# Kernel optimization log

Hardware: AMD Instinct MI355X
Metric: run time of the kernel (lower is better)

The kernel has to match this reference:

```python
import jax, jax.numpy as jnp
import numpy as np


def setup_inputs() -> dict:
    key = jax.random.key(0)
    ks = jax.random.split(key, 7)
    B, I, H, O, T = 1024, 2048, 2048, 2048, 30
    s = 1.0 / np.sqrt(H)
    return {
        "x": jax.random.normal(ks[0], (B, I), dtype=jnp.float32),
        "w_ih": jax.random.uniform(ks[1], (3 * H, I), jnp.float32, -s, s),
        "w_hh": jax.random.uniform(ks[2], (3 * H, H), jnp.float32, -s, s),
        "b_ih": jax.random.uniform(ks[3], (3 * H,), jnp.float32, -s, s),
        "b_hh": jax.random.uniform(ks[4], (3 * H,), jnp.float32, -s, s),
        "w_cls": jax.random.uniform(ks[5], (O, H), jnp.float32, -s, s),
        "b_cls": jax.random.uniform(ks[6], (O,), jnp.float32, -s, s),
        "num_timesteps": T,
    }


def reference(x, w_ih, w_hh, b_ih, b_hh, w_cls, b_cls, num_timesteps):
    # Original module never updates hidden_unit inside the loop, so every
    # timestep computes GRUCell(x, 0) -> identical output. Compute once,
    # broadcast across T (same math as the torch loop).
    # GRUCell with h=0: W_hh @ h vanishes; only bias_hh contributes.
    gi = x @ w_ih.T + b_ih                      # [B, 3H]
    i_r, i_z, i_n = jnp.split(gi, 3, axis=1)    # each [B, H]
    h_r, h_z, h_n = jnp.split(b_hh, 3)          # each [H]
    r = jax.nn.sigmoid(i_r + h_r)
    z = jax.nn.sigmoid(i_z + h_z)
    n = jnp.tanh(i_n + r * h_n)
    h_new = (1.0 - z) * n                       # + z * 0
    out = jax.nn.sigmoid(h_new @ w_cls.T + b_cls)  # [B, O]
    B, O = out.shape
    # torch stacks along dim 2 -> [B, O, T]; squeeze is a no-op for B,O,T > 1
    return jnp.broadcast_to(out[:, :, None], (B, O, num_timesteps))
```

## Files before the change

kernel.cpp:

```cpp
#include <hip/hip_runtime.h>
#include <hip/hip_bf16.h>
#include <math.h>

typedef __attribute__((ext_vector_type(8))) _Float16 f16x8;
typedef __attribute__((ext_vector_type(4))) float f32x4;

static __device__ __forceinline__ float sigmoidf_(float x) {
    return 1.0f / (1.0f + expf(-x));
}

__global__ void cvt_swz(const float* __restrict__ src, _Float16* __restrict__ dst,
                        int nchunks, int ck)
{
    const int c = blockIdx.x * 256 + threadIdx.x;
    if (c >= nchunks) return;
    const int row = c / ck;
    const int kc  = c - row * ck;
    const int kcs = (kc & ~7) | ((kc & 7) ^ (row & 7));
    const float* s = src + (size_t)c * 8;
    float4 v0 = *(const float4*)s;
    float4 v1 = *(const float4*)(s + 4);
    f16x8 h;
    h[0] = (_Float16)v0.x; h[1] = (_Float16)v0.y;
    h[2] = (_Float16)v0.z; h[3] = (_Float16)v0.w;
    h[4] = (_Float16)v1.x; h[5] = (_Float16)v1.y;
    h[6] = (_Float16)v1.z; h[7] = (_Float16)v1.w;
    *(f16x8*)(dst + (size_t)row * ((size_t)ck * 8) + (size_t)kcs * 8) = h;
}

template <int BM, int BN, int EPI>
__launch_bounds__(256, 3)
__global__ void gemm16(const _Float16* __restrict__ A, const _Float16* __restrict__ Bw,
                       const float* __restrict__ bias, float* __restrict__ C,
                       int M, int N, int K)
{
    constexpr int BK = 64;
    constexpr int WM = BM / 2, WN = BN / 2;
    constexpr int MR = WM / 16, NR = WN / 16;

    __shared__ _Float16 As[BM * BK];
    __shared__ _Float16 Bs[BN * BK];

    const int tid  = threadIdx.x;
    const int lane = tid & 63;
    const int wid  = tid >> 6;
    const int wr   = wid >> 1;
    const int wc   = wid & 1;
    const int brow = blockIdx.y * BM;
    const int bcol = blockIdx.x * BN;
    const int lr   = lane & 15;
    const int kb   = lane >> 4;

    f32x4 acc[MR][NR] = {};

    for (int k0 = 0; k0 < K; k0 += BK) {
        __syncthreads();
#pragma unroll
        for (int i = 0; i < BM * 8; i += 256) {
            const int c = tid + i;
            const _Float16* src = A + (size_t)(brow + (c >> 3)) * K + k0 + (c & 7) * 8;
            __builtin_amdgcn_global_load_lds(
                (const __attribute__((address_space(1))) void*)src,
                (__attribute__((address_space(3))) void*)&As[(size_t)(i + wid * 64) * 8],
                16, 0, 0);
        }
#pragma unroll
        for (int i = 0; i < BN * 8; i += 256) {
            const int c = tid + i;
            const _Float16* src = Bw + (size_t)(bcol + (c >> 3)) * K + k0 + (c & 7) * 8;
            __builtin_amdgcn_global_load_lds(
                (const __attribute__((address_space(1))) void*)src,
                (__attribute__((address_space(3))) void*)&Bs[(size_t)(i + wid * 64) * 8],
                16, 0, 0);
        }
        __syncthreads();

#pragma unroll
        for (int ks = 0; ks < 2; ++ks) {
            f16x8 af[MR], bf[NR];
#pragma unroll
            for (int m = 0; m < MR; ++m) {
                const int row = wr * WM + m * 16 + lr;
                const int ch  = (ks * 4 + kb) ^ (row & 7);
                af[m] = *(const f16x8*)&As[row * BK + ch * 8];
            }
#pragma unroll
            for (int n = 0; n < NR; ++n) {
                const int row = wc * WN + n * 16 + lr;
                const int ch  = (ks * 4 + kb) ^ (row & 7);
                bf[n] = *(const f16x8*)&Bs[row * BK + ch * 8];
            }
#pragma unroll
            for (int m = 0; m < MR; ++m)
#pragma unroll
                for (int n = 0; n < NR; ++n)
                    acc[m][n] = __builtin_amdgcn_mfma_f32_16x16x32_f16(af[m], bf[n], acc[m][n], 0, 0, 0);
        }
    }

#pragma unroll
    for (int m = 0; m < MR; ++m) {
        const int row0 = brow + wr * WM + m * 16 + (lane >> 4) * 4;
#pragma unroll
        for (int n = 0; n < NR; ++n) {
            const int col = bcol + wc * WN + n * 16 + lr;
            const float bv = bias[col];
#pragma unroll
            for (int j = 0; j < 4; ++j) {
                float v = acc[m][n][j] + bv;
                if (EPI) v = sigmoidf_(v);
                C[(size_t)(row0 + j) * N + col] = v;
            }
        }
    }
}

__global__ void gate_swz(const float* __restrict__ gi, const float* __restrict__ b_hh,
                         _Float16* __restrict__ hn, int B, int H)
{
    const int ch = H >> 3;
    const int c = blockIdx.x * 256 + threadIdx.x;
    if (c >= B * ch) return;
    const int b  = c / ch;
    const int hc = c - b * ch;
    const int h0 = hc * 8;
    const float* g = gi + (size_t)b * 3 * H;
    f16x8 o;
#pragma unroll
    for (int q = 0; q < 2; ++q) {
        float4 ir  = *(const float4*)(g + h0 + 4 * q);
        float4 iz  = *(const float4*)(g + H + h0 + 4 * q);
        float4 in4 = *(const float4*)(g + 2 * H + h0 + 4 * q);
        float4 hr  = *(const float4*)(b_hh + h0 + 4 * q);
        float4 hz  = *(const float4*)(b_hh + H + h0 + 4 * q);
        float4 hn4 = *(const float4*)(b_hh + 2 * H + h0 + 4 * q);
        float r, z;
        r = sigmoidf_(ir.x + hr.x); z = sigmoidf_(iz.x + hz.x);
        o[4 * q + 0] = (_Float16)((1.0f - z) * tanhf(in4.x + r * hn4.x));
        r = sigmoidf_(ir.y + hr.y); z = sigmoidf_(iz.y + hz.y);
        o[4 * q + 1] = (_Float16)((1.0f - z) * tanhf(in4.y + r * hn4.y));
        r = sigmoidf_(ir.z + hr.z); z = sigmoidf_(iz.z + hz.z);
        o[4 * q + 2] = (_Float16)((1.0f - z) * tanhf(in4.z + r * hn4.z));
        r = sigmoidf_(ir.w + hr.w); z = sigmoidf_(iz.w + hz.w);
        o[4 * q + 3] = (_Float16)((1.0f - z) * tanhf(in4.w + r * hn4.w));
    }
    const int hcs = (hc & ~7) | ((hc & 7) ^ (b & 7));
    *(f16x8*)(hn + (size_t)b * H + (size_t)hcs * 8) = o;
}

__global__ void bcast_kernel(const float* __restrict__ res,
                             float* __restrict__ out, int BO, int T)
{
    const int bo0 = blockIdx.x * 256;
    if (T & 1) {
        float* op = out + (size_t)bo0 * T;
        const int n = 256 * T;
        for (int j = threadIdx.x; j < n; j += blockDim.x)
            op[j] = res[bo0 + j / T];
    } else {
        const int half = T >> 1;
        float2* o2 = (float2*)(out + (size_t)bo0 * T);
        const int n2 = 256 * half;
        for (int j = threadIdx.x; j < n2; j += blockDim.x) {
            const float v = res[bo0 + j / half];
            o2[j] = make_float2(v, v);
        }
    }
}

extern "C" void kernel_launch(void* const* d_in, const int* in_sizes, int n_in,
                              void* d_out, int out_size, void* d_ws, size_t ws_size,
                              hipStream_t stream)
{
    const float* x     = (const float*)d_in[0];
    const float* w_ih  = (const float*)d_in[1];
    const float* b_ih  = (const float*)d_in[3];
    const float* b_hh  = (const float*)d_in[4];
    const float* w_cls = (const float*)d_in[5];
    const float* b_cls = (const float*)d_in[6];

    const int H3 = in_sizes[3];
    const int H  = H3 / 3;
    const int I  = in_sizes[1] / H3;
    const int B  = in_sizes[0] / I;
    const int O  = in_sizes[6];
    const int T  = out_size / (B * O);

    _Float16* x16    = (_Float16*)d_ws;
    _Float16* wcls16 = x16 + (size_t)B * I;
    _Float16* hn16   = wcls16 + (size_t)O * H;
    float*    res    = (float*)(hn16 + (size_t)B * H);

    char*     outc  = (char*)d_out;
    _Float16* wih16 = (_Float16*)outc;
    float*    gi    = (float*)(outc + (size_t)H3 * I * 2);
    float*    out   = (float*)d_out;

    dim3 blk(256);

    cvt_swz<<<(B * I / 8 + 255) / 256, blk, 0, stream>>>(x, x16, B * I / 8, I / 8);
    cvt_swz<<<(H3 * I / 8 + 255) / 256, blk, 0, stream>>>(w_ih, wih16, H3 * I / 8, I / 8);
    cvt_swz<<<(O * H / 8 + 255) / 256, blk, 0, stream>>>(w_cls, wcls16, O * H / 8, H / 8);

    gemm16<64, 128, 0><<<dim3(H3 / 128, B / 64), blk, 0, stream>>>(x16, wih16, b_ih, gi, B, H3, I);

    gate_swz<<<(B * H / 8 + 255) / 256, blk, 0, stream>>>(gi, b_hh, hn16, B, H);

    gemm16<64, 64, 1><<<dim3(O / 64, B / 64), blk, 0, stream>>>(hn16, wcls16, b_cls, res, B, O, H);

    bcast_kernel<<<(B * O) / 256, blk, 0, stream>>>(res, out, B * O, T);
}
```

Baseline: 408.9 us.

## Rewrite GEMMs as single-wave double-buffered kernels, fuse broadcast and conversions

The three fp32-to-fp16 conversions are merged into one launch. Both GEMMs are replaced by a single-wavefront (64-thread) kernel that double-buffers LDS tiles with async global-to-LDS loads and raises scheduling priority around the MFMA block. The intermediate gate activations are stored as fp16 to halve their traffic. The classifier GEMM epilogue writes the T-broadcast output directly, which removes the separate broadcast kernel. The trade-offs are lower occupancy per block, a wide uncoalesced strided store in the epilogue, and reduced precision on the intermediate activations.

```diff
diff --git a/kernel.cpp b/kernel.cpp
--- a/kernel.cpp
+++ b/kernel.cpp
@@ -9,113 +9,149 @@
     return 1.0f / (1.0f + expf(-x));
 }
 
-__global__ void cvt_swz(const float* __restrict__ src, _Float16* __restrict__ dst,
-                        int nchunks, int ck)
-{
-    const int c = blockIdx.x * 256 + threadIdx.x;
-    if (c >= nchunks) return;
+__global__ void cvt_all(const float* __restrict__ s0, _Float16* __restrict__ d0, int n0,
+                        const float* __restrict__ s1, _Float16* __restrict__ d1, int n1,
+                        const float* __restrict__ s2, _Float16* __restrict__ d2, int n2,
+                        int ck01, int ck2)
+{
+    int c = blockIdx.x * 256 + threadIdx.x;
+    const float* s; _Float16* d; int ck;
+    if (c < n0)            { s = s0; d = d0; ck = ck01; }
+    else if (c < n0 + n1)  { c -= n0; s = s1; d = d1; ck = ck01; }
+    else                   { c -= n0 + n1; if (c >= n2) return; s = s2; d = d2; ck = ck2; }
     const int row = c / ck;
     const int kc  = c - row * ck;
     const int kcs = (kc & ~7) | ((kc & 7) ^ (row & 7));
-    const float* s = src + (size_t)c * 8;
-    float4 v0 = *(const float4*)s;
-    float4 v1 = *(const float4*)(s + 4);
+    const float* sp = s + (size_t)c * 8;
+    float4 v0 = *(const float4*)sp;
+    float4 v1 = *(const float4*)(sp + 4);
     f16x8 h;
     h[0] = (_Float16)v0.x; h[1] = (_Float16)v0.y;
     h[2] = (_Float16)v0.z; h[3] = (_Float16)v0.w;
     h[4] = (_Float16)v1.x; h[5] = (_Float16)v1.y;
     h[6] = (_Float16)v1.z; h[7] = (_Float16)v1.w;
-    *(f16x8*)(dst + (size_t)row * ((size_t)ck * 8) + (size_t)kcs * 8) = h;
+    *(f16x8*)(d + (size_t)row * ((size_t)ck * 8) + (size_t)kcs * 8) = h;
 }
 
 template <int BM, int BN, int EPI>
-__launch_bounds__(256, 3)
-__global__ void gemm16(const _Float16* __restrict__ A, const _Float16* __restrict__ Bw,
-                       const float* __restrict__ bias, float* __restrict__ C,
-                       int M, int N, int K)
-{
-    constexpr int BK = 64;
-    constexpr int WM = BM / 2, WN = BN / 2;
-    constexpr int MR = WM / 16, NR = WN / 16;
-
-    __shared__ _Float16 As[BM * BK];
-    __shared__ _Float16 Bs[BN * BK];
+__launch_bounds__(64, 1)
+__global__ void gemm_sw(const _Float16* __restrict__ A, const _Float16* __restrict__ Bw,
+                        const float* __restrict__ bias, void* __restrict__ Cv,
+                        int N, int K, int T)
+{
+    constexpr int MR = BM / 16, NR = BN / 16;
+    constexpr int NA = BM / 8, NB = BN / 8;
+    constexpr int NL = NA + NB;
+
+    __shared__ _Float16 As[2][BM * 64];
+    __shared__ _Float16 Bs[2][BN * 64];
 
     const int tid  = threadIdx.x;
-    const int lane = tid & 63;
-    const int wid  = tid >> 6;
-    const int wr   = wid >> 1;
-    const int wc   = wid & 1;
+    const int lr   = tid & 15;
+    const int kb   = tid >> 4;
     const int brow = blockIdx.y * BM;
     const int bcol = blockIdx.x * BN;
-    const int lr   = lane & 15;
-    const int kb   = lane >> 4;
+
+    const _Float16* ap = A  + (size_t)(brow + (tid >> 3)) * K + (tid & 7) * 8;
+    const _Float16* bp = Bw + (size_t)(bcol + (tid >> 3)) * K + (tid & 7) * 8;
+
+    const int eb0 = lr * 64 + (((0 * 4 + kb) ^ (lr & 7)) * 8);
+    const int eb1 = lr * 64 + (((1 * 4 + kb) ^ (lr & 7)) * 8);
 
     f32x4 acc[MR][NR] = {};
 
-    for (int k0 = 0; k0 < K; k0 += BK) {
-        __syncthreads();
-#pragma unroll
-        for (int i = 0; i < BM * 8; i += 256) {
-            const int c = tid + i;
-            const _Float16* src = A + (size_t)(brow + (c >> 3)) * K + k0 + (c & 7) * 8;
+    auto stage = [&](int buf, int kt) {
+        const _Float16* a = ap + (size_t)kt * 64;
+#pragma unroll
+        for (int i = 0; i < NA; ++i)
             __builtin_amdgcn_global_load_lds(
-                (const __attribute__((address_space(1))) void*)src,
-                (__attribute__((address_space(3))) void*)&As[(size_t)(i + wid * 64) * 8],
+                (const __attribute__((address_space(1))) void*)(a + (size_t)i * 8 * K),
+                (__attribute__((address_space(3))) void*)&As[buf][(i * 64 + tid) * 8],
                 16, 0, 0);
-        }
-#pragma unroll
-        for (int i = 0; i < BN * 8; i += 256) {
-            const int c = tid + i;
-            const _Float16* src = Bw + (size_t)(bcol + (c >> 3)) * K + k0 + (c & 7) * 8;
+        const _Float16* b = bp + (size_t)kt * 64;
+#pragma unroll
+        for (int i = 0; i < NB; ++i)
             __builtin_amdgcn_global_load_lds(
-                (const __attribute__((address_space(1))) void*)src,
-                (__attribute__((address_space(3))) void*)&Bs[(size_t)(i + wid * 64) * 8],
+                (const __attribute__((address_space(1))) void*)(b + (size_t)i * 8 * K),
+                (__attribute__((address_space(3))) void*)&Bs[buf][(i * 64 + tid) * 8],
                 16, 0, 0);
-        }
-        __syncthreads();
-
+    };
+
+    auto compute = [&](int cur) {
+        const _Float16* as = &As[cur][0];
+        const _Float16* bs = &Bs[cur][0];
+        __builtin_amdgcn_s_setprio(1);
 #pragma unroll
         for (int ks = 0; ks < 2; ++ks) {
+            const int eb = ks ? eb1 : eb0;
             f16x8 af[MR], bf[NR];
 #pragma unroll
-            for (int m = 0; m < MR; ++m) {
-                const int row = wr * WM + m * 16 + lr;
-                const int ch  = (ks * 4 + kb) ^ (row & 7);
-                af[m] = *(const f16x8*)&As[row * BK + ch * 8];
-            }
-#pragma unroll
-            for (int n = 0; n < NR; ++n) {
-                const int row = wc * WN + n * 16 + lr;
-                const int ch  = (ks * 4 + kb) ^ (row & 7);
-                bf[n] = *(const f16x8*)&Bs[row * BK + ch * 8];
-            }
-#pragma unroll
-            for (int m = 0; m < MR; ++m)
-#pragma unroll
-                for (int n = 0; n < NR; ++n)
+            for (int m = 0; m < MR; ++m) af[m] = *(const f16x8*)(as + m * 16 * 64 + eb);
+#pragma unroll
+            for (int n = 0; n < NR; ++n) bf[n] = *(const f16x8*)(bs + n * 16 * 64 + eb);
+#pragma unroll
+            for (int n = 0; n < NR; ++n)
+#pragma unroll
+                for (int m = 0; m < MR; ++m)
                     acc[m][n] = __builtin_amdgcn_mfma_f32_16x16x32_f16(af[m], bf[n], acc[m][n], 0, 0, 0);
         }
-    }
-
-#pragma unroll
-    for (int m = 0; m < MR; ++m) {
-        const int row0 = brow + wr * WM + m * 16 + (lane >> 4) * 4;
-#pragma unroll
-        for (int n = 0; n < NR; ++n) {
-            const int col = bcol + wc * WN + n * 16 + lr;
-            const float bv = bias[col];
-#pragma unroll
-            for (int j = 0; j < 4; ++j) {
-                float v = acc[m][n][j] + bv;
-                if (EPI) v = sigmoidf_(v);
-                C[(size_t)(row0 + j) * N + col] = v;
+        __builtin_amdgcn_s_setprio(0);
+    };
+
+    const int nt = K / 64;
+    stage(0, 0);
+    int t = 0;
+    for (; t < nt - 1; ++t) {
+        stage((t & 1) ^ 1, t + 1);
+        asm volatile("s_waitcnt vmcnt(%0)" :: "i"(NL) : "memory");
+        __builtin_amdgcn_sched_barrier(0);
+        compute(t & 1);
+    }
+    asm volatile("s_waitcnt vmcnt(0)" ::: "memory");
+    __builtin_amdgcn_sched_barrier(0);
+    compute(t & 1);
+
+    if (EPI == 0) {
+        _Float16* C = (_Float16*)Cv;
+#pragma unroll
+        for (int m = 0; m < MR; ++m) {
+            const int r0 = brow + m * 16 + kb * 4;
+#pragma unroll
+            for (int n = 0; n < NR; ++n) {
+                const int col = bcol + n * 16 + lr;
+                const float bv = bias[col];
+#pragma unroll
+                for (int j = 0; j < 4; ++j)
+                    C[(size_t)(r0 + j) * N + col] = (_Float16)(acc[m][n][j] + bv);
             }
         }
-    }
-}
-
-__global__ void gate_swz(const float* __restrict__ gi, const float* __restrict__ b_hh,
+    } else {
+        float* Co = (float*)Cv;
+#pragma unroll
+        for (int m = 0; m < MR; ++m) {
+            const int r0 = brow + m * 16 + kb * 4;
+#pragma unroll
+            for (int n = 0; n < NR; ++n) {
+                const int col = bcol + n * 16 + lr;
+                const float bv = bias[col];
+#pragma unroll
+                for (int j = 0; j < 4; ++j) {
+                    const float v = sigmoidf_(acc[m][n][j] + bv);
+                    const size_t base = ((size_t)(r0 + j) * N + col) * (size_t)T;
+                    if (!(T & 1)) {
+                        float2* o2 = (float2*)(Co + base);
+                        const float2 vv = make_float2(v, v);
+                        for (int p = 0; p < T / 2; ++p) o2[p] = vv;
+                    } else {
+                        for (int p = 0; p < T; ++p) Co[base + p] = v;
+                    }
+                }
+            }
+        }
+    }
+}
+
+__global__ void gate_swz(const _Float16* __restrict__ gi, const float* __restrict__ b_hh,
                          _Float16* __restrict__ hn, int B, int H)
 {
     const int ch = H >> 3;
@@ -124,48 +160,26 @@
     const int b  = c / ch;
     const int hc = c - b * ch;
     const int h0 = hc * 8;
-    const float* g = gi + (size_t)b * 3 * H;
+    const _Float16* g = gi + (size_t)b * 3 * H + h0;
+    f16x8 ir = *(const f16x8*)g;
+    f16x8 iz = *(const f16x8*)(g + H);
+    f16x8 in = *(const f16x8*)(g + 2 * H);
+    float hr[8], hz[8], hnn[8];
+    *(float4*)&hr[0]  = *(const float4*)(b_hh + h0);
+    *(float4*)&hr[4]  = *(const float4*)(b_hh + h0 + 4);
+    *(float4*)&hz[0]  = *(const float4*)(b_hh + H + h0);
+    *(float4*)&hz[4]  = *(const float4*)(b_hh + H + h0 + 4);
+    *(float4*)&hnn[0] = *(const float4*)(b_hh + 2 * H + h0);
+    *(float4*)&hnn[4] = *(const float4*)(b_hh + 2 * H + h0 + 4);
     f16x8 o;
 #pragma unroll
-    for (int q = 0; q < 2; ++q) {
-        float4 ir  = *(const float4*)(g + h0 + 4 * q);
-        float4 iz  = *(const float4*)(g + H + h0 + 4 * q);
-        float4 in4 = *(const float4*)(g + 2 * H + h0 + 4 * q);
-        float4 hr  = *(const float4*)(b_hh + h0 + 4 * q);
-        float4 hz  = *(const float4*)(b_hh + H + h0 + 4 * q);
-        float4 hn4 = *(const float4*)(b_hh + 2 * H + h0 + 4 * q);
-        float r, z;
-        r = sigmoidf_(ir.x + hr.x); z = sigmoidf_(iz.x + hz.x);
-        o[4 * q + 0] = (_Float16)((1.0f - z) * tanhf(in4.x + r * hn4.x));
-        r = sigmoidf_(ir.y + hr.y); z = sigmoidf_(iz.y + hz.y);
-        o[4 * q + 1] = (_Float16)((1.0f - z) * tanhf(in4.y + r * hn4.y));
-        r = sigmoidf_(ir.z + hr.z); z = sigmoidf_(iz.z + hz.z);
-        o[4 * q + 2] = (_Float16)((1.0f - z) * tanhf(in4.z + r * hn4.z));
-        r = sigmoidf_(ir.w + hr.w); z = sigmoidf_(iz.w + hz.w);
-        o[4 * q + 3] = (_Float16)((1.0f - z) * tanhf(in4.w + r * hn4.w));
+    for (int q = 0; q < 8; ++q) {
+        const float r = sigmoidf_((float)ir[q] + hr[q]);
+        const float z = sigmoidf_((float)iz[q] + hz[q]);
+        o[q] = (_Float16)((1.0f - z) * tanhf((float)in[q] + r * hnn[q]));
     }
     const int hcs = (hc & ~7) | ((hc & 7) ^ (b & 7));
     *(f16x8*)(hn + (size_t)b * H + (size_t)hcs * 8) = o;
-}
-
-__global__ void bcast_kernel(const float* __restrict__ res,
-                             float* __restrict__ out, int BO, int T)
-{
-    const int bo0 = blockIdx.x * 256;
-    if (T & 1) {
-        float* op = out + (size_t)bo0 * T;
-        const int n = 256 * T;
-        for (int j = threadIdx.x; j < n; j += blockDim.x)
-            op[j] = res[bo0 + j / T];
-    } else {
-        const int half = T >> 1;
-        float2* o2 = (float2*)(out + (size_t)bo0 * T);
-        const int n2 = 256 * half;
-        for (int j = threadIdx.x; j < n2; j += blockDim.x) {
-            const float v = res[bo0 + j / half];
-            o2[j] = make_float2(v, v);
-        }
-    }
 }
 
 extern "C" void kernel_launch(void* const* d_in, const int* in_sizes, int n_in,
@@ -189,24 +203,24 @@
     _Float16* x16    = (_Float16*)d_ws;
     _Float16* wcls16 = x16 + (size_t)B * I;
     _Float16* hn16   = wcls16 + (size_t)O * H;
-    float*    res    = (float*)(hn16 + (size_t)B * H);
-
-    char*     outc  = (char*)d_out;
-    _Float16* wih16 = (_Float16*)outc;
-    float*    gi    = (float*)(outc + (size_t)H3 * I * 2);
-    float*    out   = (float*)d_out;
+
+    _Float16* wih16 = (_Float16*)d_out;
+    _Float16* gi16  = wih16 + (size_t)H3 * I;
 
     dim3 blk(256);
 
-    cvt_swz<<<(B * I / 8 + 255) / 256, blk, 0, stream>>>(x, x16, B * I / 8, I / 8);
-    cvt_swz<<<(H3 * I / 8 + 255) / 256, blk, 0, stream>>>(w_ih, wih16, H3 * I / 8, I / 8);
-    cvt_swz<<<(O * H / 8 + 255) / 256, blk, 0, stream>>>(w_cls, wcls16, O * H / 8, H / 8);
-
-    gemm16<64, 128, 0><<<dim3(H3 / 128, B / 64), blk, 0, stream>>>(x16, wih16, b_ih, gi, B, H3, I);
-
-    gate_swz<<<(B * H / 8 + 255) / 256, blk, 0, stream>>>(gi, b_hh, hn16, B, H);
-
-    gemm16<64, 64, 1><<<dim3(O / 64, B / 64), blk, 0, stream>>>(hn16, wcls16, b_cls, res, B, O, H);
-
-    bcast_kernel<<<(B * O) / 256, blk, 0, stream>>>(res, out, B * O, T);
-}
+    {
+        const int n0 = B * I / 8, n1 = H3 * I / 8, n2 = O * H / 8;
+        const int tot = n0 + n1 + n2;
+        cvt_all<<<(tot + 255) / 256, blk, 0, stream>>>(x, x16, n0, w_ih, wih16, n1,
+                                                       w_cls, wcls16, n2, I / 8, H / 8);
+    }
+
+    gemm_sw<64, 128, 0><<<dim3(H3 / 128, B / 64), dim3(64), 0, stream>>>(
+        x16, wih16, b_ih, gi16, H3, I, 0);
+
+    gate_swz<<<(B * H / 8 + 255) / 256, blk, 0, stream>>>(gi16, b_hh, hn16, B, H);
+
+    gemm_sw<64, 64, 1><<<dim3(O / 64, B / 64), dim3(64), 0, stream>>>(
+        hn16, wcls16, b_cls, d_out, O, H, T);
+}
```

Result: slower. 542.0 us (+32.5%).

## Merge weight conversions, store gate preactivations as fp16, retile first GEMM

Applied to the files above, without the earlier changes.

The three fp32-to-fp16 conversion launches become a single kernel. The first GEMM now writes its gate preactivations in fp16 rather than fp32, which halves the intermediate traffic read by the gate kernel. That GEMM also moves to 128x96 tiles with two blocks per SM, and per-iteration address math is hoisted out of the load loops. Storing the preactivations in fp16 costs some precision before the sigmoid and tanh.

```diff
diff --git a/kernel.cpp b/kernel.cpp
--- a/kernel.cpp
+++ b/kernel.cpp
@@ -9,30 +9,35 @@
     return 1.0f / (1.0f + expf(-x));
 }
 
-__global__ void cvt_swz(const float* __restrict__ src, _Float16* __restrict__ dst,
-                        int nchunks, int ck)
-{
-    const int c = blockIdx.x * 256 + threadIdx.x;
-    if (c >= nchunks) return;
+__global__ void cvt_all(const float* __restrict__ s0, _Float16* __restrict__ d0, int n0,
+                        const float* __restrict__ s1, _Float16* __restrict__ d1, int n1,
+                        const float* __restrict__ s2, _Float16* __restrict__ d2, int n2,
+                        int ck01, int ck2)
+{
+    int c = blockIdx.x * 256 + threadIdx.x;
+    const float* s; _Float16* d; int ck;
+    if (c < n0)            { s = s0; d = d0; ck = ck01; }
+    else if (c < n0 + n1)  { c -= n0; s = s1; d = d1; ck = ck01; }
+    else                   { c -= n0 + n1; if (c >= n2) return; s = s2; d = d2; ck = ck2; }
     const int row = c / ck;
     const int kc  = c - row * ck;
     const int kcs = (kc & ~7) | ((kc & 7) ^ (row & 7));
-    const float* s = src + (size_t)c * 8;
-    float4 v0 = *(const float4*)s;
-    float4 v1 = *(const float4*)(s + 4);
+    const float* sp = s + (size_t)c * 8;
+    float4 v0 = *(const float4*)sp;
+    float4 v1 = *(const float4*)(sp + 4);
     f16x8 h;
     h[0] = (_Float16)v0.x; h[1] = (_Float16)v0.y;
     h[2] = (_Float16)v0.z; h[3] = (_Float16)v0.w;
     h[4] = (_Float16)v1.x; h[5] = (_Float16)v1.y;
     h[6] = (_Float16)v1.z; h[7] = (_Float16)v1.w;
-    *(f16x8*)(dst + (size_t)row * ((size_t)ck * 8) + (size_t)kcs * 8) = h;
+    *(f16x8*)(d + (size_t)row * ((size_t)ck * 8) + (size_t)kcs * 8) = h;
 }
 
 template <int BM, int BN, int EPI>
-__launch_bounds__(256, 3)
-__global__ void gemm16(const _Float16* __restrict__ A, const _Float16* __restrict__ Bw,
-                       const float* __restrict__ bias, float* __restrict__ C,
-                       int M, int N, int K)
+__launch_bounds__(256, 2)
+__global__ void gemm_mw(const _Float16* __restrict__ A, const _Float16* __restrict__ Bw,
+                        const float* __restrict__ bias, void* __restrict__ Cv,
+                        int N, int K)
 {
     constexpr int BK = 64;
     constexpr int WM = BM / 2, WN = BN / 2;
@@ -51,28 +56,25 @@
     const int lr   = lane & 15;
     const int kb   = lane >> 4;
 
+    const _Float16* ap = A  + (size_t)(brow + (tid >> 3)) * K + (tid & 7) * 8;
+    const _Float16* bp = Bw + (size_t)(bcol + (tid >> 3)) * K + (tid & 7) * 8;
+
     f32x4 acc[MR][NR] = {};
 
     for (int k0 = 0; k0 < K; k0 += BK) {
         __syncthreads();
 #pragma unroll
-        for (int i = 0; i < BM * 8; i += 256) {
-            const int c = tid + i;
-            const _Float16* src = A + (size_t)(brow + (c >> 3)) * K + k0 + (c & 7) * 8;
+        for (int c0 = 0; c0 < BM * 8; c0 += 256)
             __builtin_amdgcn_global_load_lds(
-                (const __attribute__((address_space(1))) void*)src,
-                (__attribute__((address_space(3))) void*)&As[(size_t)(i + wid * 64) * 8],
+                (const __attribute__((address_space(1))) void*)(ap + k0 + (size_t)(c0 >> 3) * K),
+                (__attribute__((address_space(3))) void*)&As[(c0 + tid) * 8],
                 16, 0, 0);
-        }
-#pragma unroll
-        for (int i = 0; i < BN * 8; i += 256) {
-            const int c = tid + i;
-            const _Float16* src = Bw + (size_t)(bcol + (c >> 3)) * K + k0 + (c & 7) * 8;
+#pragma unroll
+        for (int c0 = 0; c0 < BN * 8; c0 += 256)
             __builtin_amdgcn_global_load_lds(
-                (const __attribute__((address_space(1))) void*)src,
-                (__attribute__((address_space(3))) void*)&Bs[(size_t)(i + wid * 64) * 8],
+                (const __attribute__((address_space(1))) void*)(bp + k0 + (size_t)(c0 >> 3) * K),
+                (__attribute__((address_space(3))) void*)&Bs[(c0 + tid) * 8],
                 16, 0, 0);
-        }
         __syncthreads();
 
 #pragma unroll
@@ -81,41 +83,41 @@
 #pragma unroll
             for (int m = 0; m < MR; ++m) {
                 const int row = wr * WM + m * 16 + lr;
-                const int ch  = (ks * 4 + kb) ^ (row & 7);
-                af[m] = *(const f16x8*)&As[row * BK + ch * 8];
+                af[m] = *(const f16x8*)&As[row * BK + ((ks * 4 + kb) ^ (row & 7)) * 8];
             }
 #pragma unroll
             for (int n = 0; n < NR; ++n) {
                 const int row = wc * WN + n * 16 + lr;
-                const int ch  = (ks * 4 + kb) ^ (row & 7);
-                bf[n] = *(const f16x8*)&Bs[row * BK + ch * 8];
+                bf[n] = *(const f16x8*)&Bs[row * BK + ((ks * 4 + kb) ^ (row & 7)) * 8];
             }
 #pragma unroll
-            for (int m = 0; m < MR; ++m)
-#pragma unroll
-                for (int n = 0; n < NR; ++n)
+            for (int n = 0; n < NR; ++n)
+#pragma unroll
+                for (int m = 0; m < MR; ++m)
                     acc[m][n] = __builtin_amdgcn_mfma_f32_16x16x32_f16(af[m], bf[n], acc[m][n], 0, 0, 0);
         }
     }
 
 #pragma unroll
     for (int m = 0; m < MR; ++m) {
-        const int row0 = brow + wr * WM + m * 16 + (lane >> 4) * 4;
+        const int r0 = brow + wr * WM + m * 16 + kb * 4;
 #pragma unroll
         for (int n = 0; n < NR; ++n) {
             const int col = bcol + wc * WN + n * 16 + lr;
             const float bv = bias[col];
 #pragma unroll
             for (int j = 0; j < 4; ++j) {
-                float v = acc[m][n][j] + bv;
-                if (EPI) v = sigmoidf_(v);
-                C[(size_t)(row0 + j) * N + col] = v;
+                const float v = acc[m][n][j] + bv;
+                if (EPI == 0)
+                    ((_Float16*)Cv)[(size_t)(r0 + j) * N + col] = (_Float16)v;
+                else
+                    ((float*)Cv)[(size_t)(r0 + j) * N + col] = sigmoidf_(v);
             }
         }
     }
 }
 
-__global__ void gate_swz(const float* __restrict__ gi, const float* __restrict__ b_hh,
+__global__ void gate_swz(const _Float16* __restrict__ gi, const float* __restrict__ b_hh,
                          _Float16* __restrict__ hn, int B, int H)
 {
     const int ch = H >> 3;
@@ -124,25 +126,23 @@
     const int b  = c / ch;
     const int hc = c - b * ch;
     const int h0 = hc * 8;
-    const float* g = gi + (size_t)b * 3 * H;
+    const _Float16* g = gi + (size_t)b * 3 * H + h0;
+    f16x8 ir = *(const f16x8*)g;
+    f16x8 iz = *(const f16x8*)(g + H);
+    f16x8 in = *(const f16x8*)(g + 2 * H);
+    float hr[8], hz[8], hnn[8];
+    *(float4*)&hr[0]  = *(const float4*)(b_hh + h0);
+    *(float4*)&hr[4]  = *(const float4*)(b_hh + h0 + 4);
+    *(float4*)&hz[0]  = *(const float4*)(b_hh + H + h0);
+    *(float4*)&hz[4]  = *(const float4*)(b_hh + H + h0 + 4);
+    *(float4*)&hnn[0] = *(const float4*)(b_hh + 2 * H + h0);
+    *(float4*)&hnn[4] = *(const float4*)(b_hh + 2 * H + h0 + 4);
     f16x8 o;
 #pragma unroll
-    for (int q = 0; q < 2; ++q) {
-        float4 ir  = *(const float4*)(g + h0 + 4 * q);
-        float4 iz  = *(const float4*)(g + H + h0 + 4 * q);
-        float4 in4 = *(const float4*)(g + 2 * H + h0 + 4 * q);
-        float4 hr  = *(const float4*)(b_hh + h0 + 4 * q);
-        float4 hz  = *(const float4*)(b_hh + H + h0 + 4 * q);
-        float4 hn4 = *(const float4*)(b_hh + 2 * H + h0 + 4 * q);
-        float r, z;
-        r = sigmoidf_(ir.x + hr.x); z = sigmoidf_(iz.x + hz.x);
-        o[4 * q + 0] = (_Float16)((1.0f - z) * tanhf(in4.x + r * hn4.x));
-        r = sigmoidf_(ir.y + hr.y); z = sigmoidf_(iz.y + hz.y);
-        o[4 * q + 1] = (_Float16)((1.0f - z) * tanhf(in4.y + r * hn4.y));
-        r = sigmoidf_(ir.z + hr.z); z = sigmoidf_(iz.z + hz.z);
-        o[4 * q + 2] = (_Float16)((1.0f - z) * tanhf(in4.z + r * hn4.z));
-        r = sigmoidf_(ir.w + hr.w); z = sigmoidf_(iz.w + hz.w);
-        o[4 * q + 3] = (_Float16)((1.0f - z) * tanhf(in4.w + r * hn4.w));
+    for (int q = 0; q < 8; ++q) {
+        const float r = sigmoidf_((float)ir[q] + hr[q]);
+        const float z = sigmoidf_((float)iz[q] + hz[q]);
+        o[q] = (_Float16)((1.0f - z) * tanhf((float)in[q] + r * hnn[q]));
     }
     const int hcs = (hc & ~7) | ((hc & 7) ^ (b & 7));
     *(f16x8*)(hn + (size_t)b * H + (size_t)hcs * 8) = o;
@@ -191,22 +191,25 @@
     _Float16* hn16   = wcls16 + (size_t)O * H;
     float*    res    = (float*)(hn16 + (size_t)B * H);
 
-    char*     outc  = (char*)d_out;
-    _Float16* wih16 = (_Float16*)outc;
-    float*    gi    = (float*)(outc + (size_t)H3 * I * 2);
-    float*    out   = (float*)d_out;
+    _Float16* wih16 = (_Float16*)d_out;
+    _Float16* gi16  = wih16 + (size_t)H3 * I;
 
     dim3 blk(256);
 
-    cvt_swz<<<(B * I / 8 + 255) / 256, blk, 0, stream>>>(x, x16, B * I / 8, I / 8);
-    cvt_swz<<<(H3 * I / 8 + 255) / 256, blk, 0, stream>>>(w_ih, wih16, H3 * I / 8, I / 8);
-    cvt_swz<<<(O * H / 8 + 255) / 256, blk, 0, stream>>>(w_cls, wcls16, O * H / 8, H / 8);
-
-    gemm16<64, 128, 0><<<dim3(H3 / 128, B / 64), blk, 0, stream>>>(x16, wih16, b_ih, gi, B, H3, I);
-
-    gate_swz<<<(B * H / 8 + 255) / 256, blk, 0, stream>>>(gi, b_hh, hn16, B, H);
-
-    gemm16<64, 64, 1><<<dim3(O / 64, B / 64), blk, 0, stream>>>(hn16, wcls16, b_cls, res, B, O, H);
-
-    bcast_kernel<<<(B * O) / 256, blk, 0, stream>>>(res, out, B * O, T);
-}
+    {
+        const int n0 = B * I / 8, n1 = H3 * I / 8, n2 = O * H / 8;
+        const int tot = n0 + n1 + n2;
+        cvt_all<<<(tot + 255) / 256, blk, 0, stream>>>(x, x16, n0, w_ih, wih16, n1,
+                                                       w_cls, wcls16, n2, I / 8, H / 8);
+    }
+
+    gemm_mw<128, 96, 0><<<dim3(H3 / 96, B / 128), blk, 0, stream>>>(
+        x16, wih16, b_ih, gi16, H3, I);
+
+    gate_swz<<<(B * H / 8 + 255) / 256, blk, 0, stream>>>(gi16, b_hh, hn16, B, H);
+
+    gemm_mw<64, 64, 1><<<dim3(O / 64, B / 64), blk, 0, stream>>>(
+        hn16, wcls16, b_cls, res, O, H);
+
+    bcast_kernel<<<(B * O) / 256, blk, 0, stream>>>(res, (float*)d_out, B * O, T);
+}
```

New measurement: 411.0 us. About the same (+0.5%).
